# Kernel tuning notes

Hardware: AMD Instinct MI355X
Metric: run time of the kernel (lower is better)

The kernel has to match this reference:

```python
import jax, jax.numpy as jnp
import numpy as np

BETA = 0.5
ITEM_NUM = 100000
REGION_NUM = 1000
EMBED = 128
HIDDEN = 256
B, H = 1024, 256


def setup_inputs() -> dict:
    key = jax.random.key(0)
    ks = jax.random.split(key, 10)
    history = jax.random.randint(ks[0], (B, H), 0, ITEM_NUM)
    target = jax.random.randint(ks[1], (B,), 0, ITEM_NUM)
    history_region = jax.random.randint(ks[2], (B, H), 0, REGION_NUM)
    target_region = jax.random.randint(ks[3], (B,), 0, REGION_NUM)
    E_hist = 0.01 * jax.random.normal(ks[4], (ITEM_NUM, EMBED), dtype=jnp.float32)
    E_targ = 0.01 * jax.random.normal(ks[5], (ITEM_NUM, EMBED), dtype=jnp.float32)
    E_reg = 0.01 * jax.random.normal(ks[6], (REGION_NUM, EMBED), dtype=jnp.float32)
    lim1 = 1.0 / np.sqrt(2 * EMBED)
    W1 = jax.random.uniform(ks[7], (2 * EMBED, HIDDEN), jnp.float32, -lim1, lim1)
    b1 = jnp.zeros((HIDDEN,), jnp.float32)
    lim2 = 1.0 / np.sqrt(HIDDEN)
    w2 = jax.random.uniform(ks[8], (HIDDEN,), jnp.float32, -lim2, lim2)
    return {"history": history, "target": target,
            "history_region": history_region, "target_region": target_region,
            "E_hist": E_hist, "E_targ": E_targ, "E_reg": E_reg,
            "W1": W1, "b1": b1, "w2": w2}


def reference(history, target, history_region, target_region,
              E_hist, E_targ, E_reg, W1, b1, w2):
    # gathers + concat: hist [B,H,2d], tgt [B,2d]
    hist = jnp.concatenate([E_hist[history], E_reg[history_region]], axis=-1)
    tgt = jnp.concatenate([E_targ[target], E_reg[target_region]], axis=-1)
    # elementwise product broadcast over history dim
    inp = hist * tgt[:, None, :]                      # [B,H,2d]
    hid = jax.nn.relu(jnp.einsum('bhd,dk->bhk', inp, W1) + b1)
    scores = jnp.einsum('bhk,k->bh', hid, w2)         # [B,H]
    mask = (history != target[:, None]).astype(scores.dtype)
    exp_a = jnp.exp(scores) * mask                    # [B,H]
    denom = jnp.power(jnp.sum(exp_a, axis=-1), BETA)  # [B]
    attn = exp_a / denom[:, None]                     # [B,H]
    # weighted reduction: sum_h sum_d hist*attn*tgt
    pred = jnp.einsum('bhd,bh,bd->b', hist, attn, tgt)
    return jax.nn.sigmoid(pred)
```

## Files before the change

### kernel.cpp

```cpp
#include <hip/hip_runtime.h>
#include <hip/hip_bf16.h>

#define NB 1024
#define NH 256
#define EMB 128
#define TWOD 256
#define HID 256
#define ROWS 128
#define BPB 2
#define NBLK (NB * BPB)

typedef __attribute__((ext_vector_type(4))) float f32x4;
typedef __attribute__((ext_vector_type(8))) short bf16x8;

__device__ __forceinline__ unsigned short f2bf(float f) {
  union { float f; unsigned u; } v; v.f = f;
  unsigned u = v.u;
  unsigned r = (u + 0x7fffu + ((u >> 16) & 1u)) >> 16;
  return (unsigned short)r;
}

__global__ __launch_bounds__(256) void prep_w1t(const float* __restrict__ W1,
                                                unsigned short* __restrict__ W1T) {
  const int bx = blockIdx.x & 3;
  const int by = blockIdx.x >> 2;
  __shared__ float tile[64][65];
  const int tr = threadIdx.x >> 6;
  const int tc = threadIdx.x & 63;
  #pragma unroll
  for (int i = 0; i < 16; ++i) {
    const int d = bx * 64 + i * 4 + tr;
    tile[i * 4 + tr][tc] = W1[(size_t)d * HID + by * 64 + tc];
  }
  __syncthreads();
  #pragma unroll
  for (int i = 0; i < 16; ++i) {
    const int n = by * 64 + i * 4 + tr;
    W1T[(size_t)n * TWOD + bx * 64 + tc] = f2bf(tile[tc][i * 4 + tr]);
  }
}

__global__ __launch_bounds__(512, 4) void nais_main(
    const int* __restrict__ history, const int* __restrict__ target,
    const int* __restrict__ hregion, const int* __restrict__ tregion,
    const float* __restrict__ E_hist, const float* __restrict__ E_targ,
    const float* __restrict__ E_reg,
    const unsigned short* __restrict__ W1T, const float* __restrict__ b1,
    const float* __restrict__ w2,
    float* __restrict__ part_se, float* __restrict__ part_sd)
{
  const int blk = blockIdx.x;
  const int b = blk >> 1;
  const int r0 = (blk & 1) * ROWS;
  const int tid = threadIdx.x;
  const int lane = tid & 63;
  const int wave = tid >> 6;
  const int l15 = lane & 15;
  const int lhi = lane >> 4;
  const int l31 = lane & 31;
  const int halfsel = lane >> 5;

  __shared__ __align__(16) unsigned short inp_lds[ROWS * 256];
  __shared__ float dot_lds[ROWS];
  __shared__ int items_lds[ROWS];
  __shared__ float score_parts[8][ROWS];

  const float* tsrc = halfsel ? (E_reg + (size_t)tregion[b] * EMB)
                              : (E_targ + (size_t)target[b] * EMB);
  const f32x4 t = *(const f32x4*)(tsrc + l31 * 4);
  const int tgt_item = target[b];

  const int* keysrc = halfsel ? hregion : history;
  const float* table = halfsel ? E_reg : E_hist;

  {
    int key[16];
    #pragma unroll
    for (int s = 0; s < 16; ++s)
      key[s] = keysrc[b * NH + r0 + wave * 16 + s];

    #pragma unroll
    for (int pass = 0; pass < 2; ++pass) {
      f32x4 vb[8];
      #pragma unroll
      for (int s = 0; s < 8; ++s)
        vb[s] = *(const f32x4*)(table + (size_t)key[pass * 8 + s] * EMB + l31 * 4);

      #pragma unroll
      for (int s = 0; s < 8; ++s) {
        const int row = wave * 16 + pass * 8 + s;
        if (lane == 0) items_lds[row] = key[pass * 8 + s];
        f32x4 v = vb[s] * t;
        float2 f01; f01.x = v[0]; f01.y = v[1];
        float2 f23; f23.x = v[2]; f23.y = v[3];
        __hip_bfloat162 p0 = __float22bfloat162_rn(f01);
        __hip_bfloat162 p1 = __float22bfloat162_rn(f23);
        union { __hip_bfloat162 h; unsigned u; } c0, c1;
        c0.h = p0; c1.h = p1;
        const int g = halfsel * 16 + (l31 >> 1);
        const int gs = g ^ (row & 7) ^ ((g >> 3) & 3);
        unsigned* dst = (unsigned*)&inp_lds[row * 256 + gs * 8 + (lane & 1) * 4];
        dst[0] = c0.u; dst[1] = c1.u;
      }
    }
  }
  __syncthreads();

  {
    const int col0 = wave * 32;
    float b1v[2], w2v[2];
    #pragma unroll
    for (int n = 0; n < 2; ++n) {
      const int colh = col0 + n * 16 + l15;
      b1v[n] = b1[colh];
      w2v[n] = w2[colh];
    }

    f32x4 acc[2][4][2];
    #pragma unroll
    for (int c = 0; c < 2; ++c)
      #pragma unroll
      for (int m = 0; m < 4; ++m)
        #pragma unroll
        for (int n = 0; n < 2; ++n)
          acc[c][m][n] = (f32x4){0.f, 0.f, 0.f, 0.f};

    #pragma unroll
    for (int kk = 0; kk < 8; ++kk) {
      bf16x8 bfr[2];
      #pragma unroll
      for (int n = 0; n < 2; ++n) {
        const int colh = col0 + n * 16 + l15;
        bfr[n] = *(const bf16x8*)(W1T + (size_t)colh * TWOD + kk * 32 + lhi * 8);
      }
      bf16x8 af[2][4];
      #pragma unroll
      for (int c = 0; c < 2; ++c)
        #pragma unroll
        for (int m = 0; m < 4; ++m) {
          const int row = c * 64 + m * 16 + l15;
          const int gk = kk * 4 + lhi;
          const int gs = gk ^ (row & 7) ^ ((gk >> 3) & 3);
          af[c][m] = *(const bf16x8*)(&inp_lds[row * 256 + gs * 8]);
        }
      __builtin_amdgcn_s_setprio(1);
      #pragma unroll
      for (int c = 0; c < 2; ++c)
        #pragma unroll
        for (int m = 0; m < 4; ++m)
          #pragma unroll
          for (int n = 0; n < 2; ++n)
            acc[c][m][n] = __builtin_amdgcn_mfma_f32_16x16x32_bf16(af[c][m], bfr[n], acc[c][m][n], 0, 0, 0);
      __builtin_amdgcn_s_setprio(0);
    }

    {
      const int drow = wave * 16 + (lane >> 2);
      const int seg = lane & 3;
      float dsum = 0.f;
      #pragma unroll
      for (int j = 0; j < 8; ++j) {
        const int gidx = seg * 8 + ((j + drow) & 7);
        const int gs = gidx ^ (drow & 7) ^ (seg & 3);
        union { bf16x8 w; unsigned u[4]; } a;
        a.w = *(const bf16x8*)(&inp_lds[drow * 256 + gs * 8]);
        #pragma unroll
        for (int q = 0; q < 4; ++q) {
          union { unsigned u; float f; } lo, hi;
          lo.u = a.u[q] << 16;
          hi.u = a.u[q] & 0xFFFF0000u;
          dsum += lo.f + hi.f;
        }
      }
      dsum += __shfl_xor(dsum, 1);
      dsum += __shfl_xor(dsum, 2);
      if (seg == 0) dot_lds[drow] = dsum;
    }

    #pragma unroll
    for (int c = 0; c < 2; ++c) {
      #pragma unroll
      for (int m = 0; m < 4; ++m) {
        #pragma unroll
        for (int r = 0; r < 4; ++r) {
          float p = 0.f;
          #pragma unroll
          for (int n = 0; n < 2; ++n) {
            float hv = acc[c][m][n][r] + b1v[n];
            hv = hv > 0.f ? hv : 0.f;
            p += hv * w2v[n];
          }
          p += __shfl_xor(p, 1);
          p += __shfl_xor(p, 2);
          p += __shfl_xor(p, 4);
          p += __shfl_xor(p, 8);
          if (l15 == 0) score_parts[wave][c * 64 + m * 16 + lhi * 4 + r] = p;
        }
      }
    }
  }
  __syncthreads();

  if (wave < 2) {
    const int lrow = wave * 64 + lane;
    float sc = 0.f;
    #pragma unroll
    for (int w = 0; w < 8; ++w) sc += score_parts[w][lrow];
    float e = (items_lds[lrow] != tgt_item) ? expf(sc) : 0.f;
    float ed = e * dot_lds[lrow];
    #pragma unroll
    for (int off = 32; off >= 1; off >>= 1) {
      e += __shfl_xor(e, off);
      ed += __shfl_xor(ed, off);
    }
    if (lane == 0) {
      part_se[blk * 2 + wave] = e;
      part_sd[blk * 2 + wave] = ed;
    }
  }
}

__global__ __launch_bounds__(256) void finalize(const float* __restrict__ part_se,
                                                const float* __restrict__ part_sd,
                                                float* __restrict__ out) {
  const int b = blockIdx.x * 256 + threadIdx.x;
  if (b < NB) {
    float se = 0.f, sd = 0.f;
    #pragma unroll
    for (int i = 0; i < BPB * 2; ++i) {
      se += part_se[b * BPB * 2 + i];
      sd += part_sd[b * BPB * 2 + i];
    }
    const float pred = (se > 0.f) ? (sd / sqrtf(se)) : 0.f;
    out[b] = 1.f / (1.f + expf(-pred));
  }
}

extern "C" void kernel_launch(void* const* d_in, const int* in_sizes, int n_in,
                              void* d_out, int out_size, void* d_ws, size_t ws_size,
                              hipStream_t stream) {
  const int* history = (const int*)d_in[0];
  const int* target  = (const int*)d_in[1];
  const int* hregion = (const int*)d_in[2];
  const int* tregion = (const int*)d_in[3];
  const float* E_hist = (const float*)d_in[4];
  const float* E_targ = (const float*)d_in[5];
  const float* E_reg  = (const float*)d_in[6];
  const float* W1 = (const float*)d_in[7];
  const float* b1 = (const float*)d_in[8];
  const float* w2 = (const float*)d_in[9];
  float* out = (float*)d_out;

  char* p = (char*)d_ws;
  unsigned short* W1T = (unsigned short*)p;  p += (size_t)TWOD * HID * 2;
  float* part_se = (float*)p;                p += (size_t)NBLK * 2 * 4;
  float* part_sd = (float*)p;

  prep_w1t<<<16, 256, 0, stream>>>(W1, W1T);
  nais_main<<<NBLK, 512, 0, stream>>>(history, target, hregion, tregion,
                                      E_hist, E_targ, E_reg, W1T, b1, w2,
                                      part_se, part_sd);
  finalize<<<(NB + 255) / 256, 256, 0, stream>>>(part_se, part_sd, out);
}
```

Baseline: 86.09 us.

## Stream history embeddings directly into LDS via global_load_lds, then convert in place

After: 85.69 us. No clear change (-0.5%).

```diff
diff --git a/kernel.cpp b/kernel.cpp
--- a/kernel.cpp
+++ b/kernel.cpp
@@ -58,50 +58,73 @@
   const int l15 = lane & 15;
   const int lhi = lane >> 4;
   const int l31 = lane & 31;
-  const int halfsel = lane >> 5;
 
   __shared__ __align__(16) unsigned short inp_lds[ROWS * 256];
   __shared__ float dot_lds[ROWS];
-  __shared__ int items_lds[ROWS];
+  __shared__ int keys_h[ROWS];
+  __shared__ int keys_r[ROWS];
   __shared__ float score_parts[8][ROWS];
 
-  const float* tsrc = halfsel ? (E_reg + (size_t)tregion[b] * EMB)
-                              : (E_targ + (size_t)target[b] * EMB);
-  const f32x4 t = *(const f32x4*)(tsrc + l31 * 4);
   const int tgt_item = target[b];
 
-  const int* keysrc = halfsel ? hregion : history;
-  const float* table = halfsel ? E_reg : E_hist;
+  if (tid < ROWS) {
+    keys_h[tid] = history[b * NH + r0 + tid];
+  } else if (tid < 2 * ROWS) {
+    keys_r[tid - ROWS] = hregion[b * NH + r0 + (tid - ROWS)];
+  }
+  __syncthreads();
 
   {
-    int key[16];
-    #pragma unroll
-    for (int s = 0; s < 16; ++s)
-      key[s] = keysrc[b * NH + r0 + wave * 16 + s];
-
-    #pragma unroll
-    for (int pass = 0; pass < 2; ++pass) {
-      f32x4 vb[8];
-      #pragma unroll
-      for (int s = 0; s < 8; ++s)
-        vb[s] = *(const f32x4*)(table + (size_t)key[pass * 8 + s] * EMB + l31 * 4);
-
-      #pragma unroll
-      for (int s = 0; s < 8; ++s) {
-        const int row = wave * 16 + pass * 8 + s;
-        if (lane == 0) items_lds[row] = key[pass * 8 + s];
-        f32x4 v = vb[s] * t;
-        float2 f01; f01.x = v[0]; f01.y = v[1];
-        float2 f23; f23.x = v[2]; f23.y = v[3];
-        __hip_bfloat162 p0 = __float22bfloat162_rn(f01);
-        __hip_bfloat162 p1 = __float22bfloat162_rn(f23);
-        union { __hip_bfloat162 h; unsigned u; } c0, c1;
-        c0.h = p0; c1.h = p1;
-        const int g = halfsel * 16 + (l31 >> 1);
-        const int gs = g ^ (row & 7) ^ ((g >> 3) & 3);
-        unsigned* dst = (unsigned*)&inp_lds[row * 256 + gs * 8 + (lane & 1) * 4];
-        dst[0] = c0.u; dst[1] = c1.u;
-      }
+    #pragma unroll
+    for (int i = 0; i < 8; ++i) {
+      const int wr0 = wave * 16 + i * 2;
+      const int kh = keys_h[wr0 + (lane >> 5)];
+      const float* src = E_hist + (size_t)kh * EMB + (lane & 31) * 4;
+      __builtin_amdgcn_global_load_lds(
+          (const __attribute__((address_space(1))) void*)src,
+          (__attribute__((address_space(3))) void*)&inp_lds[wr0 * 256],
+          16, 0, 0);
+    }
+
+    const f32x4 t4r = *(const f32x4*)(E_reg + (size_t)tregion[b] * EMB + l31 * 4);
+    f32x4 vb[8];
+    #pragma unroll
+    for (int i = 0; i < 8; ++i) {
+      const int rr = wave * 16 + i * 2 + (lane >> 5);
+      vb[i] = *(const f32x4*)(E_reg + (size_t)keys_r[rr] * EMB + l31 * 4);
+    }
+
+    const float2 t2h = *(const float2*)(E_targ + (size_t)tgt_item * EMB + lane * 2);
+
+    asm volatile("s_waitcnt vmcnt(0)" ::: "memory");
+    __builtin_amdgcn_sched_barrier(0);
+
+    #pragma unroll
+    for (int s = 0; s < 16; ++s) {
+      const int row = wave * 16 + s;
+      const char* rbase = (const char*)&inp_lds[row * 256];
+      float2 f = *(const float2*)(rbase + lane * 8);
+      float2 v; v.x = f.x * t2h.x; v.y = f.y * t2h.y;
+      union { __hip_bfloat162 h; unsigned u; } c;
+      c.h = __float22bfloat162_rn(v);
+      const int g = lane >> 2;
+      const int gs = g ^ (row & 7) ^ ((g >> 3) & 3);
+      *(unsigned*)((char*)&inp_lds[row * 256] + gs * 16 + (lane & 3) * 4) = c.u;
+    }
+
+    #pragma unroll
+    for (int i = 0; i < 8; ++i) {
+      const int row = wave * 16 + i * 2 + (lane >> 5);
+      f32x4 v = vb[i] * t4r;
+      float2 f01; f01.x = v[0]; f01.y = v[1];
+      float2 f23; f23.x = v[2]; f23.y = v[3];
+      union { __hip_bfloat162 h; unsigned u; } c0, c1;
+      c0.h = __float22bfloat162_rn(f01);
+      c1.h = __float22bfloat162_rn(f23);
+      const int g = 16 + (l31 >> 1);
+      const int gs = g ^ (row & 7) ^ ((g >> 3) & 3);
+      unsigned* dst = (unsigned*)((char*)&inp_lds[row * 256] + gs * 16 + (l31 & 1) * 8);
+      dst[0] = c0.u; dst[1] = c1.u;
     }
   }
   __syncthreads();
@@ -206,7 +229,7 @@
     float sc = 0.f;
     #pragma unroll
     for (int w = 0; w < 8; ++w) sc += score_parts[w][lrow];
-    float e = (items_lds[lrow] != tgt_item) ? expf(sc) : 0.f;
+    float e = (keys_h[lrow] != tgt_item) ? expf(sc) : 0.f;
     float ed = e * dot_lds[lrow];
     #pragma unroll
     for (int off = 32; off >= 1; off >>= 1) {
```
